# Optimization experiments

Measured on AMD Instinct MI355X. Metric: run time of the kernel, lower is better.

## Reference

```python
import jax, jax.numpy as jnp
import numpy as np

EPS = 1e-5

def _layer_norm(x, w, b):
    mu = jnp.mean(x, axis=-1, keepdims=True)
    var = jnp.mean((x - mu) ** 2, axis=-1, keepdims=True)
    return (x - mu) * jax.lax.rsqrt(var + EPS) * w + b

B, N, C, D = 8, 16384, 256, 2
K = 4096  # ceil(N / 4)

def setup_inputs() -> dict:
    key = jax.random.key(0)
    k0, k1, k2, k3 = jax.random.split(key, 4)
    pos = jax.random.uniform(k0, (B, N, D), dtype=jnp.float32)
    feat = jax.random.normal(k1, (B, N, C), dtype=jnp.float32)
    assignment = jax.random.randint(k2, (B, N), 0, K)
    norm_w = jnp.ones((C + D,), jnp.float32)
    norm_b = jnp.zeros((C + D,), jnp.float32)
    lin_w = jax.random.normal(k3, (2 * C, C + D), jnp.float32) * 0.02
    return {"pos": pos, "feat": feat, "assignment": assignment,
            "norm_w": norm_w, "norm_b": norm_b, "lin_w": lin_w}

def reference(pos, feat, assignment, norm_w, norm_b, lin_w):
    b, n, c = feat.shape
    d = pos.shape[2]
    k = K
    # normalize coordinates by per-dim global max
    pos = pos / jnp.max(pos.reshape(-1, d), axis=0)
    # flatten (batch, cluster) into segments for one big segment_sum
    seg = (assignment + jnp.arange(b, dtype=assignment.dtype)[:, None] * k).reshape(-1)  # [b*n]
    count = jax.ops.segment_sum(jnp.ones((b * n,), pos.dtype), seg,
                                num_segments=b * k).reshape(b, k)
    safe = jnp.maximum(count, 1.0)
    # cluster mean position (scatter_add + divide)
    mean_pos = jax.ops.segment_sum(pos.reshape(-1, d), seg,
                                   num_segments=b * k).reshape(b, k, d) / safe[..., None]
    # relative position via gather
    idx = jnp.broadcast_to(assignment[:, :, None], (b, n, d))
    rel_pos = pos - jnp.take_along_axis(mean_pos, idx, axis=1)
    # norm + linear (dim+pos_dim -> 2*dim, no bias)
    h = _layer_norm(jnp.concatenate([feat, rel_pos], axis=-1), norm_w, norm_b)
    h = jnp.einsum('bnf,of->bno', h, lin_w)  # [b, n, 2c]
    # cluster mean pooling of features (segment sum / count)
    merged = jax.ops.segment_sum(h.reshape(b * n, 2 * c), seg,
                                 num_segments=b * k).reshape(b, k, 2 * c) / safe[..., None]
    # zero out empty clusters and emit validity mask (valid_row_idx path)
    valid = (count > 0).astype(merged.dtype)  # [b, k]
    new_feat = merged * valid[..., None]
    new_pos = mean_pos * valid[..., None]
    new_mask = valid[..., None]  # [b, k, 1]
    return (new_pos, new_feat, new_mask)
```

## Files before the change

kernel.cpp:

```cpp
#include <hip/hip_runtime.h>

#define BB 8
#define NN 16384
#define CC 256
#define KK 4096
#define FDIM 258
#define FP 320
#define OC 512
#define NPTS (BB * NN)
#define NROWS (BB * KK)
#define CAP 64
#define LNEPS 1e-5f

#define OUT_FEAT_OFF 65536
#define OUT_MASK_OFF (65536 + 16777216)

#define OFF_MAX 0
#define OFF_ICOUNT 16
#define MEMSET_FLOATS (16 + NROWS)
#define OFF_ACCH 32784
#define ACC_FSLOTS (NROWS * FP / 2)
#define OFF_INV (OFF_ACCH + ACC_FSLOTS)
#define OFF_LIST (OFF_INV + NROWS)
#define OFF_WPH (OFF_LIST + NROWS * CAP)

typedef _Float16 h8v __attribute__((ext_vector_type(8)));
typedef _Float16 h4v __attribute__((ext_vector_type(4)));
typedef float f4v __attribute__((ext_vector_type(4)));

#define PREP_PB 512
#define PREP_WB 160

__global__ __launch_bounds__(256) void k_prep(const float* __restrict__ pos,
                                              const int* __restrict__ asg,
                                              const float* __restrict__ lw,
                                              float* ws) {
    int bid = blockIdx.x;
    if (bid < PREP_PB) {
        int i = bid * 256 + threadIdx.x;
        int* icount = (int*)(ws + OFF_ICOUNT);
        int* list = (int*)(ws + OFF_LIST);
        float2 p = ((const float2*)pos)[i];
        int b = i >> 14;
        int row = b * KK + asg[i];
        int slot = atomicAdd(icount + row, 1);
        if (slot < CAP) list[row * CAP + slot] = i;
        float mx = p.x, my = p.y;
        for (int off = 32; off > 0; off >>= 1) {
            mx = fmaxf(mx, __shfl_down(mx, off));
            my = fmaxf(my, __shfl_down(my, off));
        }
        if ((threadIdx.x & 63) == 0) {
            atomicMax((int*)(ws + OFF_MAX + 0), __float_as_int(mx));
            atomicMax((int*)(ws + OFF_MAX + 1), __float_as_int(my));
        }
    } else {
        _Float16* Wh = (_Float16*)(ws + OFF_WPH);
        int e = ((bid - PREP_PB) * 256 + threadIdx.x) * 4;
        int o = e / FP, f = e - o * FP;
        h4v h;
#pragma unroll
        for (int u = 0; u < 4; ++u)
            h[u] = (f + u < FDIM) ? (_Float16)lw[o * FDIM + f + u] : (_Float16)0.f;
        *(h4v*)(Wh + e) = h;
    }
}

__global__ __launch_bounds__(256) void k_gather(
    const float* __restrict__ feat, const float* __restrict__ pos,
    const float* __restrict__ nw, const float* __restrict__ nb,
    float* ws, float* __restrict__ out) {
    int t = threadIdx.x;
    int lane = t & 63;
    int bswz = ((blockIdx.x & 7) << 10) + (blockIdx.x >> 3);
    int row = (bswz << 2) + (t >> 6);
    int q = lane >> 4;
    int ll = lane & 15;
    const int* icount = (const int*)(ws + OFF_ICOUNT);
    const int* list = (const int*)(ws + OFF_LIST);
    _Float16* Ah = (_Float16*)(ws + OFF_ACCH);

    int cnt = icount[row];
    if (cnt > CAP) cnt = CAP;
    float fcnt = (float)cnt;
    float invc = 1.f / fmaxf(fcnt, 1.f);
    float mxx = ws[OFF_MAX + 0], mxy = ws[OFF_MAX + 1];

    int ptl = (lane < cnt) ? list[row * CAP + lane] : 0;
    float px = 0.f, py = 0.f;
    if (lane < cnt) {
        float2 p = ((const float2*)pos)[ptl];
        px = p.x / mxx;
        py = p.y / mxy;
    }
    float sx = px, sy = py;
    for (int m = 32; m; m >>= 1) {
        sx += __shfl_xor(sx, m);
        sy += __shfl_xor(sy, m);
    }
    float meanx = sx * invc, meany = sy * invc;
    float valid = (cnt > 0) ? 1.f : 0.f;
    if (lane == 0) {
        out[2 * row + 0] = meanx * valid;
        out[2 * row + 1] = meany * valid;
        out[OUT_MASK_OFF + row] = valid;
        ws[OFF_INV + row] = invc;
    }

    float4 a0 = {0.f, 0.f, 0.f, 0.f}, a1 = {0.f, 0.f, 0.f, 0.f};
    float4 a2 = {0.f, 0.f, 0.f, 0.f}, a3 = {0.f, 0.f, 0.f, 0.f};
    float arx = 0.f, ary = 0.f;
    for (int s0 = 0; s0 < cnt; s0 += 4) {
        int s = s0 + q;
        int pt = __shfl(ptl, s);
        float rx = __shfl(px, s) - meanx;
        float ry = __shfl(py, s) - meany;
        const float4* fr = (const float4*)(feat + (size_t)pt * CC);
        float4 v0 = fr[ll];
        float4 v1 = fr[16 + ll];
        float4 v2 = fr[32 + ll];
        float4 v3 = fr[48 + ll];
        float S = (v0.x + v0.y + v0.z + v0.w) + (v1.x + v1.y + v1.z + v1.w) +
                  (v2.x + v2.y + v2.z + v2.w) + (v3.x + v3.y + v3.z + v3.w);
        float Q = v0.x * v0.x + v0.y * v0.y + v0.z * v0.z + v0.w * v0.w +
                  v1.x * v1.x + v1.y * v1.y + v1.z * v1.z + v1.w * v1.w +
                  v2.x * v2.x + v2.y * v2.y + v2.z * v2.z + v2.w * v2.w +
                  v3.x * v3.x + v3.y * v3.y + v3.z * v3.z + v3.w * v3.w;
        for (int m = 1; m < 16; m <<= 1) {
            S += __shfl_xor(S, m);
            Q += __shfl_xor(Q, m);
        }
        S += rx + ry;
        Q += rx * rx + ry * ry;
        float mu = S * (1.f / FDIM);
        float var = Q * (1.f / FDIM) - mu * mu;
        float w = (s < cnt) ? rsqrtf(var + LNEPS) : 0.f;
        a0.x += (v0.x - mu) * w; a0.y += (v0.y - mu) * w;
        a0.z += (v0.z - mu) * w; a0.w += (v0.w - mu) * w;
        a1.x += (v1.x - mu) * w; a1.y += (v1.y - mu) * w;
        a1.z += (v1.z - mu) * w; a1.w += (v1.w - mu) * w;
        a2.x += (v2.x - mu) * w; a2.y += (v2.y - mu) * w;
        a2.z += (v2.z - mu) * w; a2.w += (v2.w - mu) * w;
        a3.x += (v3.x - mu) * w; a3.y += (v3.y - mu) * w;
        a3.z += (v3.z - mu) * w; a3.w += (v3.w - mu) * w;
        arx += (rx - mu) * w;
        ary += (ry - mu) * w;
    }
#define MRG(x)                  \
    x += __shfl_xor(x, 16);     \
    x += __shfl_xor(x, 32);
    MRG(a0.x) MRG(a0.y) MRG(a0.z) MRG(a0.w)
    MRG(a1.x) MRG(a1.y) MRG(a1.z) MRG(a1.w)
    MRG(a2.x) MRG(a2.y) MRG(a2.z) MRG(a2.w)
    MRG(a3.x) MRG(a3.y) MRG(a3.z) MRG(a3.w)
    MRG(arx) MRG(ary)
#undef MRG

    float4 w4 = ((const float4*)nw)[lane];
    float4 b4 = ((const float4*)nb)[lane];
    float4 aq = (q == 0) ? a0 : (q == 1) ? a1 : (q == 2) ? a2 : a3;
    h4v h;
    h[0] = (_Float16)(aq.x * w4.x + fcnt * b4.x);
    h[1] = (_Float16)(aq.y * w4.y + fcnt * b4.y);
    h[2] = (_Float16)(aq.z * w4.z + fcnt * b4.z);
    h[3] = (_Float16)(aq.w * w4.w + fcnt * b4.w);
    *(h4v*)(Ah + (size_t)row * FP + lane * 4) = h;
    if (lane >= 16 && lane < 32) {
        h4v z = {};
        if (lane == 16) {
            z[0] = (_Float16)(arx * nw[256] + fcnt * nb[256]);
            z[1] = (_Float16)(ary * nw[257] + fcnt * nb[257]);
        }
        *(h4v*)(Ah + (size_t)row * FP + 256 + (lane - 16) * 4) = z;
    }
}

#define GM 128
#define GN 128
#define GK 64

__global__ __launch_bounds__(256) void k_gemm(const float* __restrict__ ws,
                                              float* __restrict__ out) {
    __shared__ _Float16 As[GM][GK];
    __shared__ _Float16 Bs[GN][GK];
    const _Float16* Ah = (const _Float16*)(ws + OFF_ACCH);
    const _Float16* Wh = (const _Float16*)(ws + OFF_WPH);
    const float* inv = ws + OFF_INV;

    int t = threadIdx.x;
    int lane = t & 63;
    int wv = t >> 6;
    int wr = wv & 1, wc = wv >> 1;
    int wg = blockIdx.x;
    int idx = wg >> 3;
    int rowtile = ((wg & 7) << 5) + (idx >> 2);
    int row0 = rowtile * GM;
    int col0 = (idx & 3) * GN;
    int l15 = lane & 15, kq = lane >> 4;
    int sw = l15 & 7;

    f4v acc[4][4] = {};

    for (int k0 = 0; k0 < FP; k0 += GK) {
#pragma unroll
        for (int l = 0; l < 4; ++l) {
            int c = l * 256 + t;
            int r = c >> 3, ch = c & 7;
            int pc = ch ^ (r & 7);
            *(uint4*)&As[r][pc * 8] = *(const uint4*)(Ah + (size_t)(row0 + r) * FP + k0 + ch * 8);
            *(uint4*)&Bs[r][pc * 8] = *(const uint4*)(Wh + (size_t)(col0 + r) * FP + k0 + ch * 8);
        }
        __syncthreads();
#pragma unroll
        for (int ks = 0; ks < 2; ++ks) {
            h8v af[4], bf[4];
            int lc = ((ks << 2) | kq);
#pragma unroll
            for (int i = 0; i < 4; ++i)
                af[i] = *(const h8v*)&As[wr * 64 + i * 16 + l15][(lc ^ sw) * 8];
#pragma unroll
            for (int j = 0; j < 4; ++j)
                bf[j] = *(const h8v*)&Bs[wc * 64 + j * 16 + l15][(lc ^ sw) * 8];
#pragma unroll
            for (int i = 0; i < 4; ++i)
#pragma unroll
                for (int j = 0; j < 4; ++j)
                    acc[i][j] = __builtin_amdgcn_mfma_f32_16x16x32_f16(
                        af[i], bf[j], acc[i][j], 0, 0, 0);
        }
        __syncthreads();
    }

#pragma unroll
    for (int i = 0; i < 4; ++i) {
#pragma unroll
        for (int r = 0; r < 4; ++r) {
            int row = row0 + wr * 64 + i * 16 + kq * 4 + r;
            float sc = inv[row];
#pragma unroll
            for (int j = 0; j < 4; ++j) {
                int col = col0 + wc * 64 + j * 16 + l15;
                out[OUT_FEAT_OFF + (size_t)row * OC + col] = acc[i][j][r] * sc;
            }
        }
    }
}

extern "C" void kernel_launch(void* const* d_in, const int* in_sizes, int n_in,
                              void* d_out, int out_size, void* d_ws, size_t ws_size,
                              hipStream_t stream) {
    const float* pos = (const float*)d_in[0];
    const float* feat = (const float*)d_in[1];
    const int* asg = (const int*)d_in[2];
    const float* nw = (const float*)d_in[3];
    const float* nb = (const float*)d_in[4];
    const float* lw = (const float*)d_in[5];
    float* out = (float*)d_out;
    float* ws = (float*)d_ws;

    hipMemsetAsync(d_ws, 0, (size_t)MEMSET_FLOATS * sizeof(float), stream);
    k_prep<<<PREP_PB + PREP_WB, 256, 0, stream>>>(pos, asg, lw, ws);
    k_gather<<<NROWS / 4, 256, 0, stream>>>(feat, pos, nw, nb, ws, out);
    k_gemm<<<NROWS / GM * (OC / GN), 256, 0, stream>>>(ws, out);
}
```

Measured before the change: 307.4 us.

## Drop padded K tail; apply rel-pos columns as rank-2 epilogue, load via global_load_lds

Shrinks the GEMM reduction dimension from 320 padded columns to 256 by pulling the two relative-position features out of the fp16 matrix. Their contribution is added in the epilogue as a rank-2 fp32 update using per-row stored values and per-column weights. The shared-memory tile loads now use direct global-to-LDS loads instead of register staging. This cuts GEMM work and traffic by about a fifth and keeps the position terms in fp32, at the cost of extra epilogue loads and a more complex prep kernel.

```diff
diff --git a/kernel.cpp b/kernel.cpp
--- a/kernel.cpp
+++ b/kernel.cpp
@@ -5,7 +5,7 @@
 #define CC 256
 #define KK 4096
 #define FDIM 258
-#define FP 320
+#define FP 256
 #define OC 512
 #define NPTS (BB * NN)
 #define NROWS (BB * KK)
@@ -23,13 +23,15 @@
 #define OFF_INV (OFF_ACCH + ACC_FSLOTS)
 #define OFF_LIST (OFF_INV + NROWS)
 #define OFF_WPH (OFF_LIST + NROWS * CAP)
+#define OFF_RP (OFF_WPH + OC * FP / 2)
+#define OFF_WC (OFF_RP + NROWS * 2)
 
 typedef _Float16 h8v __attribute__((ext_vector_type(8)));
 typedef _Float16 h4v __attribute__((ext_vector_type(4)));
 typedef float f4v __attribute__((ext_vector_type(4)));
 
 #define PREP_PB 512
-#define PREP_WB 160
+#define PREP_WB 129
 
 __global__ __launch_bounds__(256) void k_prep(const float* __restrict__ pos,
                                               const int* __restrict__ asg,
@@ -54,15 +56,21 @@
             atomicMax((int*)(ws + OFF_MAX + 0), __float_as_int(mx));
             atomicMax((int*)(ws + OFF_MAX + 1), __float_as_int(my));
         }
+    } else if (bid < PREP_PB + 128) {
+        _Float16* Wh = (_Float16*)(ws + OFF_WPH);
+        int e = (bid - PREP_PB) * 1024 + threadIdx.x * 4;
+        int o = e >> 8, f = e & 255;
+        h4v h;
+#pragma unroll
+        for (int u = 0; u < 4; ++u) h[u] = (_Float16)lw[o * FDIM + f + u];
+        *(h4v*)(Wh + e) = h;
     } else {
-        _Float16* Wh = (_Float16*)(ws + OFF_WPH);
-        int e = ((bid - PREP_PB) * 256 + threadIdx.x) * 4;
-        int o = e / FP, f = e - o * FP;
-        h4v h;
-#pragma unroll
-        for (int u = 0; u < 4; ++u)
-            h[u] = (f + u < FDIM) ? (_Float16)lw[o * FDIM + f + u] : (_Float16)0.f;
-        *(h4v*)(Wh + e) = h;
+        int o = threadIdx.x;
+        ws[OFF_WC + o] = lw[o * FDIM + 256];
+        ws[OFF_WC + 512 + o] = lw[o * FDIM + 257];
+        o += 256;
+        ws[OFF_WC + o] = lw[o * FDIM + 256];
+        ws[OFF_WC + 512 + o] = lw[o * FDIM + 257];
     }
 }
 
@@ -146,8 +154,8 @@
         arx += (rx - mu) * w;
         ary += (ry - mu) * w;
     }
-#define MRG(x)                  \
-    x += __shfl_xor(x, 16);     \
+#define MRG(x)              \
+    x += __shfl_xor(x, 16); \
     x += __shfl_xor(x, 32);
     MRG(a0.x) MRG(a0.y) MRG(a0.z) MRG(a0.w)
     MRG(a1.x) MRG(a1.y) MRG(a1.z) MRG(a1.w)
@@ -165,13 +173,9 @@
     h[2] = (_Float16)(aq.z * w4.z + fcnt * b4.z);
     h[3] = (_Float16)(aq.w * w4.w + fcnt * b4.w);
     *(h4v*)(Ah + (size_t)row * FP + lane * 4) = h;
-    if (lane >= 16 && lane < 32) {
-        h4v z = {};
-        if (lane == 16) {
-            z[0] = (_Float16)(arx * nw[256] + fcnt * nb[256]);
-            z[1] = (_Float16)(ary * nw[257] + fcnt * nb[257]);
-        }
-        *(h4v*)(Ah + (size_t)row * FP + 256 + (lane - 16) * 4) = z;
+    if (lane == 0) {
+        ws[OFF_RP + 2 * row + 0] = arx * nw[256] + fcnt * nb[256];
+        ws[OFF_RP + 2 * row + 1] = ary * nw[257] + fcnt * nb[257];
     }
 }
 
@@ -181,11 +185,12 @@
 
 __global__ __launch_bounds__(256) void k_gemm(const float* __restrict__ ws,
                                               float* __restrict__ out) {
-    __shared__ _Float16 As[GM][GK];
-    __shared__ _Float16 Bs[GN][GK];
+    __shared__ __align__(16) _Float16 As[GM * GK];
+    __shared__ __align__(16) _Float16 Bs[GN * GK];
     const _Float16* Ah = (const _Float16*)(ws + OFF_ACCH);
     const _Float16* Wh = (const _Float16*)(ws + OFF_WPH);
     const float* inv = ws + OFF_INV;
+    const float* rp = ws + OFF_RP;
 
     int t = threadIdx.x;
     int lane = t & 63;
@@ -205,10 +210,17 @@
 #pragma unroll
         for (int l = 0; l < 4; ++l) {
             int c = l * 256 + t;
-            int r = c >> 3, ch = c & 7;
-            int pc = ch ^ (r & 7);
-            *(uint4*)&As[r][pc * 8] = *(const uint4*)(Ah + (size_t)(row0 + r) * FP + k0 + ch * 8);
-            *(uint4*)&Bs[r][pc * 8] = *(const uint4*)(Wh + (size_t)(col0 + r) * FP + k0 + ch * 8);
+            int r = c >> 3;
+            int ch = (c & 7) ^ (r & 7);
+            int lb = (l * 256 + wv * 64) * 8;
+            __builtin_amdgcn_global_load_lds(
+                (const __attribute__((address_space(1))) void*)(
+                    Ah + (size_t)(row0 + r) * FP + k0 + ch * 8),
+                (__attribute__((address_space(3))) void*)(As + lb), 16, 0, 0);
+            __builtin_amdgcn_global_load_lds(
+                (const __attribute__((address_space(1))) void*)(
+                    Wh + (size_t)(col0 + r) * FP + k0 + ch * 8),
+                (__attribute__((address_space(3))) void*)(Bs + lb), 16, 0, 0);
         }
         __syncthreads();
 #pragma unroll
@@ -217,10 +229,10 @@
             int lc = ((ks << 2) | kq);
 #pragma unroll
             for (int i = 0; i < 4; ++i)
-                af[i] = *(const h8v*)&As[wr * 64 + i * 16 + l15][(lc ^ sw) * 8];
+                af[i] = *(const h8v*)&As[(wr * 64 + i * 16 + l15) * GK + ((lc ^ sw) * 8)];
 #pragma unroll
             for (int j = 0; j < 4; ++j)
-                bf[j] = *(const h8v*)&Bs[wc * 64 + j * 16 + l15][(lc ^ sw) * 8];
+                bf[j] = *(const h8v*)&Bs[(wc * 64 + j * 16 + l15) * GK + ((lc ^ sw) * 8)];
 #pragma unroll
             for (int i = 0; i < 4; ++i)
 #pragma unroll
@@ -231,16 +243,25 @@
         __syncthreads();
     }
 
+    float w0[4], w1[4];
+#pragma unroll
+    for (int j = 0; j < 4; ++j) {
+        int col = col0 + wc * 64 + j * 16 + l15;
+        w0[j] = ws[OFF_WC + col];
+        w1[j] = ws[OFF_WC + 512 + col];
+    }
 #pragma unroll
     for (int i = 0; i < 4; ++i) {
 #pragma unroll
         for (int r = 0; r < 4; ++r) {
             int row = row0 + wr * 64 + i * 16 + kq * 4 + r;
             float sc = inv[row];
+            float r0 = rp[2 * row], r1 = rp[2 * row + 1];
 #pragma unroll
             for (int j = 0; j < 4; ++j) {
                 int col = col0 + wc * 64 + j * 16 + l15;
-                out[OUT_FEAT_OFF + (size_t)row * OC + col] = acc[i][j][r] * sc;
+                out[OUT_FEAT_OFF + (size_t)row * OC + col] =
+                    (acc[i][j][r] + r0 * w0[j] + r1 * w1[j]) * sc;
             }
         }
     }
```

Result: no change. 303.1 us (median of 2 runs) (-1.4%).
